# Kernel tuning notes

Hardware: AMD Instinct MI355X
Metric: run time of the kernel (lower is better)

## Reference

```python
import jax, jax.numpy as jnp
import numpy as np

EPS = 1e-8


def _cdist(a, b):
    # a: [B,N,3], b: [B,M,3] -> euclidean distances [B,N,M]
    a2 = jnp.sum(a * a, axis=-1)[:, :, None]          # [B,N,1]
    b2 = jnp.sum(b * b, axis=-1)[:, None, :]          # [B,1,M]
    ab = jnp.einsum('bnd,bmd->bnm', a, b)             # [B,N,M]
    d2 = jnp.maximum(a2 + b2 - 2.0 * ab, 0.0)
    return jnp.sqrt(d2)


def setup_inputs() -> dict:
    key = jax.random.key(0)
    ks = jax.random.split(key, 8)
    B, N, M, C1, C2 = 16, 4096, 1024, 128, 256
    Cin = C1 + C2  # 384
    H1, H2 = 256, 128
    return {
        'xyz1': jax.random.normal(ks[0], (B, N, 3), dtype=jnp.float32),
        'xyz2': jax.random.normal(ks[1], (B, M, 3), dtype=jnp.float32),
        'points1': jax.random.normal(ks[2], (B, C1, N), dtype=jnp.float32),
        'points2': jax.random.normal(ks[3], (B, C2, M), dtype=jnp.float32),
        'W1': jax.random.normal(ks[4], (H1, Cin), dtype=jnp.float32) * (1.0 / np.sqrt(Cin)),
        'b1': jnp.zeros((H1,), dtype=jnp.float32),
        'W2': jax.random.normal(ks[5], (H2, H1), dtype=jnp.float32) * (1.0 / np.sqrt(H1)),
        'b2': jnp.zeros((H2,), dtype=jnp.float32),
    }


def reference(xyz1, xyz2, points1, points2, W1, b1, W2, b2):
    # inverse-distance weighted interpolation over ALL M source points
    dist = _cdist(xyz1, xyz2) + EPS                   # [B,N,M]
    inv = 1.0 / dist
    weight = inv / jnp.sum(inv, axis=-1, keepdims=True)
    # interpolated features: [B,N,M] @ [B,M,C2] -> [B,C2,N]
    interpolated = jnp.einsum('bnm,bcm->bcn', weight, points2)
    new_points = jnp.concatenate([points1, interpolated], axis=1)  # [B,C1+C2,N]
    # 1x1 Conv1d MLP with ReLU
    h = jax.nn.relu(jnp.einsum('oc,bcn->bon', W1, new_points) + b1[None, :, None])
    out = jax.nn.relu(jnp.einsum('oc,bcn->bon', W2, h) + b2[None, :, None])
    return out
```

## Files before the change

### kernel.cpp

```cpp
#include <hip/hip_runtime.h>
#include <math.h>

#define BBATCH 16
#define NPTS   4096
#define MPTS   1024
#define C1c    128
#define C2c    256
#define CINc   384
#define H1c    256
#define H2c    128
#define TN     64

typedef _Float16 f16x8 __attribute__((ext_vector_type(8)));
typedef _Float16 f16x4 __attribute__((ext_vector_type(4)));
typedef float    f32x4 __attribute__((ext_vector_type(4)));

#define INV_HALF   8192
#define SMEM_UNION 32768
#define SMEM_BYTES (SMEM_UNION + 1024)

#define NFRAG_P2  (BBATCH * 32 * 16 * 64)
#define NFRAG_W1  (16 * 12 * 64)
#define NFRAG_W2  (8 * 8 * 64)
#define WS_P2S  0
#define WS_W1S  (NFRAG_P2 * 8)
#define WS_W2S  (WS_W1S + NFRAG_W1 * 8)
#define WS_F16_TOTAL (WS_W2S + NFRAG_W2 * 8)

__global__ __launch_bounds__(256) void cvt_swz(
    const float* __restrict__ p2, const float* __restrict__ W1,
    const float* __restrict__ W2, _Float16* __restrict__ ws)
{
    const int t = blockIdx.x * 256 + threadIdx.x;
    const float* src;
    _Float16* dst;
    if (t < NFRAG_P2) {
        const int lane = t & 63, wt = (t >> 6) & 15, s = (t >> 10) & 31, b = t >> 15;
        const int c = wt * 16 + (lane & 15);
        const int m = s * 32 + (lane >> 4) * 8;
        src = p2 + ((size_t)(b * C2c + c)) * MPTS + m;
        dst = ws + WS_P2S + (size_t)t * 8;
    } else if (t < NFRAG_P2 + NFRAG_W1) {
        const int u = t - NFRAG_P2;
        const int lane = u & 63, kc = (u >> 6) % 12, wt = (u >> 6) / 12;
        const int o = wt * 16 + (lane & 15);
        const int k = kc * 32 + (lane >> 4) * 8;
        src = W1 + (size_t)o * CINc + k;
        dst = ws + WS_W1S + (size_t)u * 8;
    } else {
        const int v = t - NFRAG_P2 - NFRAG_W1;
        const int lane = v & 63, oc = (v >> 6) & 7, wt2 = v >> 9;
        const int o = wt2 * 16 + (lane & 15);
        const int k = oc * 32 + (lane >> 4) * 8;
        src = W2 + (size_t)o * H1c + k;
        dst = ws + WS_W2S + (size_t)v * 8;
    }
    const float4 a0 = *(const float4*)(src);
    const float4 a1 = *(const float4*)(src + 4);
    f16x8 h;
    h[0] = (_Float16)a0.x; h[1] = (_Float16)a0.y; h[2] = (_Float16)a0.z; h[3] = (_Float16)a0.w;
    h[4] = (_Float16)a1.x; h[5] = (_Float16)a1.y; h[6] = (_Float16)a1.z; h[7] = (_Float16)a1.w;
    *(f16x8*)dst = h;
}

template <bool F16P>
__global__ __launch_bounds__(256, 4) void fp_mfma8(
    const float* __restrict__ xyz1, const float* __restrict__ xyz2,
    const float* __restrict__ p1,   const float* __restrict__ p2,
    const float* __restrict__ W1,   const float* __restrict__ b1v,
    const float* __restrict__ W2,   const float* __restrict__ b2v,
    const _Float16* __restrict__ p2s, const _Float16* __restrict__ W1s,
    const _Float16* __restrict__ W2s,
    float* __restrict__ out)
{
    __shared__ __align__(16) char smem[SMEM_BYTES];
    _Float16* s_inv = (_Float16*)smem;
    _Float16* s_X   = (_Float16*)smem;
    _Float16* s_H   = (_Float16*)smem;
    float*    s_red = (float*)(smem + SMEM_UNION);

    const int tid  = threadIdx.x;
    const int w    = tid >> 6;
    const int L    = tid & 63;
    const int quad = L >> 4;
    const int l16  = L & 15;

    const int id = blockIdx.x;
    const int b  = (id & 7) * 2 + ((id >> 3) & 1);
    const int n0 = (id >> 4) * TN;

    const float* __restrict__ z2b = xyz2 + (size_t)b * MPTS * 3;
    const float* __restrict__ p2b = p2   + (size_t)b * C2c * MPTS;
    const _Float16* __restrict__ p2sb =
        F16P ? (p2s + (((size_t)b * 32 * 16 + (size_t)w * 4) * 64 + L) * 8) : (const _Float16*)nullptr;

    const float x1x = xyz1[((size_t)b * NPTS + n0 + L) * 3 + 0];
    const float x1y = xyz1[((size_t)b * NPTS + n0 + L) * 3 + 1];
    const float x1z = xyz1[((size_t)b * NPTS + n0 + L) * 3 + 2];

    f32x4 acc[4][4];
    #pragma unroll
    for (int ct = 0; ct < 4; ++ct)
        #pragma unroll
        for (int nt = 0; nt < 4; ++nt)
            acc[ct][nt] = (f32x4){0.f, 0.f, 0.f, 0.f};

    float ssum = 0.f;
    f16x8 Aa[2][4];

    auto loadA = [&](int s, f16x8 dst[4]) {
        if (F16P) {
            const _Float16* ap = p2sb + (size_t)s * (16 * 64 * 8);
            #pragma unroll
            for (int ct = 0; ct < 4; ++ct)
                dst[ct] = *(const f16x8*)(ap + (size_t)ct * (64 * 8));
        } else {
            const float* ap = p2b + (size_t)(w * 64 + l16) * MPTS + s * 32 + quad * 8;
            #pragma unroll
            for (int ct = 0; ct < 4; ++ct) {
                const float4 a0 = *(const float4*)(ap + (size_t)ct * (16 * MPTS));
                const float4 a1 = *(const float4*)(ap + (size_t)ct * (16 * MPTS) + 4);
                f16x8 h;
                h[0] = (_Float16)a0.x; h[1] = (_Float16)a0.y; h[2] = (_Float16)a0.z; h[3] = (_Float16)a0.w;
                h[4] = (_Float16)a1.x; h[5] = (_Float16)a1.y; h[6] = (_Float16)a1.z; h[7] = (_Float16)a1.w;
                dst[ct] = h;
            }
        }
    };

    auto gen = [&](int ss_) {
        _Float16* buf = s_inv + (ss_ & 1) * INV_HALF;
        const float* zbase = z2b + (size_t)(ss_ * 128 + w * 32) * 3;
        #pragma unroll
        for (int g = 0; g < 4; ++g) {
            const float* zp = zbase + g * 24;
            f32x4 zr[6];
            #pragma unroll
            for (int j = 0; j < 6; ++j) zr[j] = ((const f32x4*)zp)[j];
            const float* zv = (const float*)zr;
            f16x8 iv;
            #pragma unroll
            for (int i = 0; i < 8; ++i) {
                const float dx = x1x - zv[3 * i + 0];
                const float dy = x1y - zv[3 * i + 1];
                const float dz = x1z - zv[3 * i + 2];
                const float d2 = fmaf(dx, dx, fmaf(dy, dy, fmaf(dz, dz, 1e-12f)));
                const float inv = __builtin_amdgcn_rsqf(d2);
                ssum += inv;
                iv[i] = (_Float16)inv;
            }
            *(f16x8*)(buf + (((w * 4 + quad) * 64) + g * 16 + l16) * 8) = iv;
        }
    };

    loadA(0, Aa[0]);
    gen(0);
    __syncthreads();

    for (int ss = 0; ss < 8; ++ss) {
        if (ss + 1 < 8) gen(ss + 1);
        const _Float16* buf = s_inv + (ss & 1) * INV_HALF;
        #pragma unroll
        for (int cc = 0; cc < 4; ++cc) {
            const int s = ss * 4 + cc;
            if (s + 1 < 32) loadA(s + 1, Aa[(cc + 1) & 1]);
            #pragma unroll
            for (int nt = 0; nt < 4; ++nt) {
                const f16x8 bf = *(const f16x8*)(buf + ((cc * 4 + nt) * 64 + L) * 8);
                #pragma unroll
                for (int ct = 0; ct < 4; ++ct)
                    acc[ct][nt] = __builtin_amdgcn_mfma_f32_16x16x32_f16(Aa[cc & 1][ct], bf, acc[ct][nt], 0, 0, 0);
            }
        }
        __syncthreads();
    }

    s_red[tid] = ssum;
    __syncthreads();
    if (tid < 64)
        s_red[tid] = 1.0f / (s_red[tid] + s_red[tid + 64] + s_red[tid + 128] + s_red[tid + 192]);
    __syncthreads();

    {
        float rn4[4];
        #pragma unroll
        for (int nt = 0; nt < 4; ++nt) rn4[nt] = s_red[nt * 16 + l16];
        #pragma unroll
        for (int ct = 0; ct < 4; ++ct) {
            const int kq = 2 * w + (ct >> 1);
            const int lp = l16 + 16 * (((ct & 1) * 2) + (quad >> 1));
            const int jo = (quad & 1) * 4;
            #pragma unroll
            for (int nt = 0; nt < 4; ++nt) {
                const f32x4 v = acc[ct][nt];
                const float r = rn4[nt];
                f16x4 hv;
                hv[0] = (_Float16)(v[0] * r);
                hv[1] = (_Float16)(v[1] * r);
                hv[2] = (_Float16)(v[2] * r);
                hv[3] = (_Float16)(v[3] * r);
                *(f16x4*)(s_X + ((kq * 4 + nt) * 64 + lp) * 8 + jo) = hv;
            }
        }
    }
    __syncthreads();

    f32x4 hacc[4][4];
    #pragma unroll
    for (int ct = 0; ct < 4; ++ct)
        #pragma unroll
        for (int nt = 0; nt < 4; ++nt)
            hacc[ct][nt] = (f32x4){0.f, 0.f, 0.f, 0.f};

    {
        const float* p1f = p1 + ((size_t)b * C1c + quad * 8) * NPTS + n0 + l16;
        #pragma unroll
        for (int kc = 0; kc < 4; ++kc) {
            f16x8 af[4];
            if (F16P) {
                const _Float16* wp = W1s + (((size_t)(w * 4) * 12 + kc) * 64 + L) * 8;
                #pragma unroll
                for (int ct = 0; ct < 4; ++ct)
                    af[ct] = *(const f16x8*)(wp + (size_t)ct * (12 * 64 * 8));
            } else {
                const float* wp = W1 + (size_t)(w * 64 + l16) * CINc + kc * 32 + quad * 8;
                #pragma unroll
                for (int ct = 0; ct < 4; ++ct) {
                    const float4 a0 = *(const float4*)(wp + ct * (16 * CINc));
                    const float4 a1 = *(const float4*)(wp + ct * (16 * CINc) + 4);
                    f16x8 h;
                    h[0] = (_Float16)a0.x; h[1] = (_Float16)a0.y; h[2] = (_Float16)a0.z; h[3] = (_Float16)a0.w;
                    h[4] = (_Float16)a1.x; h[5] = (_Float16)a1.y; h[6] = (_Float16)a1.z; h[7] = (_Float16)a1.w;
                    af[ct] = h;
                }
            }
            #pragma unroll
            for (int nt = 0; nt < 4; ++nt) {
                const float* pp = p1f + (size_t)(kc * 32) * NPTS + nt * 16;
                float t[8];
                #pragma unroll
                for (int j = 0; j < 8; ++j) t[j] = pp[(size_t)j * NPTS];
                f16x8 bf;
                #pragma unroll
                for (int j = 0; j < 8; ++j) bf[j] = (_Float16)t[j];
                #pragma unroll
                for (int ct = 0; ct < 4; ++ct)
                    hacc[ct][nt] = __builtin_amdgcn_mfma_f32_16x16x32_f16(af[ct], bf, hacc[ct][nt], 0, 0, 0);
            }
        }
    }

    #pragma unroll 2
    for (int kc = 4; kc < 12; ++kc) {
        f16x8 af[4];
        if (F16P) {
            const _Float16* wp = W1s + (((size_t)(w * 4) * 12 + kc) * 64 + L) * 8;
            #pragma unroll
            for (int ct = 0; ct < 4; ++ct)
                af[ct] = *(const f16x8*)(wp + (size_t)ct * (12 * 64 * 8));
        } else {
            const float* wp = W1 + (size_t)(w * 64 + l16) * CINc + kc * 32 + quad * 8;
            #pragma unroll
            for (int ct = 0; ct < 4; ++ct) {
                const float4 a0 = *(const float4*)(wp + ct * (16 * CINc));
                const float4 a1 = *(const float4*)(wp + ct * (16 * CINc) + 4);
                f16x8 h;
                h[0] = (_Float16)a0.x; h[1] = (_Float16)a0.y; h[2] = (_Float16)a0.z; h[3] = (_Float16)a0.w;
                h[4] = (_Float16)a1.x; h[5] = (_Float16)a1.y; h[6] = (_Float16)a1.z; h[7] = (_Float16)a1.w;
                af[ct] = h;
            }
        }
        #pragma unroll
        for (int nt = 0; nt < 4; ++nt) {
            const f16x8 bf = *(const f16x8*)(s_X + (((kc - 4) * 4 + nt) * 64 + L) * 8);
            #pragma unroll
            for (int ct = 0; ct < 4; ++ct)
                hacc[ct][nt] = __builtin_amdgcn_mfma_f32_16x16x32_f16(af[ct], bf, hacc[ct][nt], 0, 0, 0);
        }
    }

    __syncthreads();

    {
        f32x4 bb[4];
        #pragma unroll
        for (int ct = 0; ct < 4; ++ct)
            bb[ct] = *(const f32x4*)(b1v + w * 64 + ct * 16 + quad * 4);
        #pragma unroll
        for (int ct = 0; ct < 4; ++ct) {
            const int oq = 2 * w + (ct >> 1);
            const int lp = l16 + 16 * (((ct & 1) * 2) + (quad >> 1));
            const int jo = (quad & 1) * 4;
            #pragma unroll
            for (int nt = 0; nt < 4; ++nt) {
                const f32x4 v = hacc[ct][nt];
                f16x4 hv;
                hv[0] = (_Float16)fmaxf(v[0] + bb[ct][0], 0.f);
                hv[1] = (_Float16)fmaxf(v[1] + bb[ct][1], 0.f);
                hv[2] = (_Float16)fmaxf(v[2] + bb[ct][2], 0.f);
                hv[3] = (_Float16)fmaxf(v[3] + bb[ct][3], 0.f);
                *(f16x4*)(s_H + ((oq * 4 + nt) * 64 + lp) * 8 + jo) = hv;
            }
        }
    }
    __syncthreads();

    f32x4 oacc[2][4];
    #pragma unroll
    for (int ct = 0; ct < 2; ++ct)
        #pragma unroll
        for (int nt = 0; nt < 4; ++nt)
            oacc[ct][nt] = (f32x4){0.f, 0.f, 0.f, 0.f};

    #pragma unroll 2
    for (int oc = 0; oc < 8; ++oc) {
        f16x8 af2[2];
        if (F16P) {
            const _Float16* wp = W2s + (((size_t)(w * 2) * 8 + oc) * 64 + L) * 8;
            #pragma unroll
            for (int ct = 0; ct < 2; ++ct)
                af2[ct] = *(const f16x8*)(wp + (size_t)ct * (8 * 64 * 8));
        } else {
            const float* wp = W2 + (size_t)(w * 32 + l16) * H1c + oc * 32 + quad * 8;
            #pragma unroll
            for (int ct = 0; ct < 2; ++ct) {
                const float4 a0 = *(const float4*)(wp + ct * (16 * H1c));
                const float4 a1 = *(const float4*)(wp + ct * (16 * H1c) + 4);
                f16x8 h;
                h[0] = (_Float16)a0.x; h[1] = (_Float16)a0.y; h[2] = (_Float16)a0.z; h[3] = (_Float16)a0.w;
                h[4] = (_Float16)a1.x; h[5] = (_Float16)a1.y; h[6] = (_Float16)a1.z; h[7] = (_Float16)a1.w;
                af2[ct] = h;
            }
        }
        #pragma unroll
        for (int nt = 0; nt < 4; ++nt) {
            const f16x8 bf = *(const f16x8*)(s_H + ((oc * 4 + nt) * 64 + L) * 8);
            #pragma unroll
            for (int ct = 0; ct < 2; ++ct)
                oacc[ct][nt] = __builtin_amdgcn_mfma_f32_16x16x32_f16(af2[ct], bf, oacc[ct][nt], 0, 0, 0);
        }
    }

    {
        f32x4 bb2[2];
        #pragma unroll
        for (int ct = 0; ct < 2; ++ct)
            bb2[ct] = *(const f32x4*)(b2v + w * 32 + ct * 16 + quad * 4);
        #pragma unroll
        for (int ct = 0; ct < 2; ++ct)
            #pragma unroll
            for (int nt = 0; nt < 4; ++nt) {
                float* op = out + ((size_t)b * H2c + w * 32 + ct * 16 + quad * 4) * NPTS
                                + n0 + nt * 16 + l16;
                #pragma unroll
                for (int j = 0; j < 4; ++j)
                    op[(size_t)j * NPTS] = fmaxf(oacc[ct][nt][j] + bb2[ct][j], 0.f);
            }
    }
}

extern "C" void kernel_launch(void* const* d_in, const int* in_sizes, int n_in,
                              void* d_out, int out_size, void* d_ws, size_t ws_size,
                              hipStream_t stream) {
    (void)in_sizes; (void)n_in; (void)out_size;
    const float* xyz1 = (const float*)d_in[0];
    const float* xyz2 = (const float*)d_in[1];
    const float* p1   = (const float*)d_in[2];
    const float* p2   = (const float*)d_in[3];
    const float* W1   = (const float*)d_in[4];
    const float* b1   = (const float*)d_in[5];
    const float* W2   = (const float*)d_in[6];
    const float* b2   = (const float*)d_in[7];
    float* out = (float*)d_out;

    dim3 grid(BBATCH * (NPTS / TN));
    dim3 block(256);
    if (ws_size >= (size_t)WS_F16_TOTAL * 2) {
        _Float16* ws = (_Float16*)d_ws;
        const int nswz = NFRAG_P2 + NFRAG_W1 + NFRAG_W2;
        cvt_swz<<<dim3(nswz / 256), dim3(256), 0, stream>>>(p2, W1, W2, ws);
        fp_mfma8<true><<<grid, block, 0, stream>>>(xyz1, xyz2, p1, p2, W1, b1, W2, b2,
                                                   ws + WS_P2S, ws + WS_W1S, ws + WS_W2S, out);
    } else {
        fp_mfma8<false><<<grid, block, 0, stream>>>(xyz1, xyz2, p1, p2, W1, b1, W2, b2,
                                                    nullptr, nullptr, nullptr, out);
    }
}
```

Measured before the change: 186.3 us.

## Stage xyz2 in LDS, stage points1 in LDS, add MFMA priority hints

Each block now copies the batch's full xyz2 (12 KB) into shared memory and the distance generation reads it from there instead of global memory. points1 is converted to fp16 and written into the shared X tile next to the interpolated features, so the first MLP layer becomes one uniform 12-chunk loop over shared memory instead of strided global loads feeding the MFMAs. s_setprio is raised around the MFMA loops. The extra ~16 KB of shared memory lowers occupancy, with launch bounds dropping from 4 to 3 blocks per CU, and adds an extra barrier.

```diff
diff --git a/kernel.cpp b/kernel.cpp
--- a/kernel.cpp
+++ b/kernel.cpp
@@ -16,8 +16,9 @@
 typedef float    f32x4 __attribute__((ext_vector_type(4)));
 
 #define INV_HALF   8192
-#define SMEM_UNION 32768
-#define SMEM_BYTES (SMEM_UNION + 1024)
+#define OFF_XYZ2   32768
+#define OFF_RED    49152
+#define SMEM_BYTES 50176
 
 #define NFRAG_P2  (BBATCH * 32 * 16 * 64)
 #define NFRAG_W1  (16 * 12 * 64)
@@ -64,7 +65,7 @@
 }
 
 template <bool F16P>
-__global__ __launch_bounds__(256, 4) void fp_mfma8(
+__global__ __launch_bounds__(256, 3) void fp_mfma9(
     const float* __restrict__ xyz1, const float* __restrict__ xyz2,
     const float* __restrict__ p1,   const float* __restrict__ p2,
     const float* __restrict__ W1,   const float* __restrict__ b1v,
@@ -74,10 +75,11 @@
     float* __restrict__ out)
 {
     __shared__ __align__(16) char smem[SMEM_BYTES];
-    _Float16* s_inv = (_Float16*)smem;
-    _Float16* s_X   = (_Float16*)smem;
-    _Float16* s_H   = (_Float16*)smem;
-    float*    s_red = (float*)(smem + SMEM_UNION);
+    _Float16* s_inv  = (_Float16*)smem;
+    float*    s_xyz2 = (float*)(smem + OFF_XYZ2);
+    _Float16* s_X    = (_Float16*)smem;
+    _Float16* s_H    = (_Float16*)smem;
+    float*    s_red  = (float*)(smem + OFF_RED);
 
     const int tid  = threadIdx.x;
     const int w    = tid >> 6;
@@ -93,6 +95,9 @@
     const float* __restrict__ p2b = p2   + (size_t)b * C2c * MPTS;
     const _Float16* __restrict__ p2sb =
         F16P ? (p2s + (((size_t)b * 32 * 16 + (size_t)w * 4) * 64 + L) * 8) : (const _Float16*)nullptr;
+
+    for (int i = tid; i < MPTS * 3 / 4; i += 256)
+        ((f32x4*)s_xyz2)[i] = ((const f32x4*)z2b)[i];
 
     const float x1x = xyz1[((size_t)b * NPTS + n0 + L) * 3 + 0];
     const float x1y = xyz1[((size_t)b * NPTS + n0 + L) * 3 + 1];
@@ -130,7 +135,7 @@
 
     auto gen = [&](int ss_) {
         _Float16* buf = s_inv + (ss_ & 1) * INV_HALF;
-        const float* zbase = z2b + (size_t)(ss_ * 128 + w * 32) * 3;
+        const float* zbase = s_xyz2 + (size_t)(ss_ * 128 + w * 32) * 3;
         #pragma unroll
         for (int g = 0; g < 4; ++g) {
             const float* zp = zbase + g * 24;
@@ -154,6 +159,7 @@
     };
 
     loadA(0, Aa[0]);
+    __syncthreads();
     gen(0);
     __syncthreads();
 
@@ -164,6 +170,7 @@
         for (int cc = 0; cc < 4; ++cc) {
             const int s = ss * 4 + cc;
             if (s + 1 < 32) loadA(s + 1, Aa[(cc + 1) & 1]);
+            __builtin_amdgcn_s_setprio(1);
             #pragma unroll
             for (int nt = 0; nt < 4; ++nt) {
                 const f16x8 bf = *(const f16x8*)(buf + ((cc * 4 + nt) * 64 + L) * 8);
@@ -171,8 +178,23 @@
                 for (int ct = 0; ct < 4; ++ct)
                     acc[ct][nt] = __builtin_amdgcn_mfma_f32_16x16x32_f16(Aa[cc & 1][ct], bf, acc[ct][nt], 0, 0, 0);
             }
+            __builtin_amdgcn_s_setprio(0);
         }
         __syncthreads();
+    }
+
+    {
+        const float* p1b = p1 + ((size_t)b * C1c + w * 32 + quad * 8) * NPTS + n0 + l16;
+        #pragma unroll
+        for (int cc = 0; cc < 4; ++cc) {
+            float t[8];
+            #pragma unroll
+            for (int j = 0; j < 8; ++j) t[j] = p1b[(size_t)j * NPTS + cc * 16];
+            f16x8 v;
+            #pragma unroll
+            for (int j = 0; j < 8; ++j) v[j] = (_Float16)t[j];
+            *(f16x8*)(s_X + ((w * 4 + cc) * 64 + L) * 8) = v;
+        }
     }
 
     s_red[tid] = ssum;
@@ -187,7 +209,7 @@
         for (int nt = 0; nt < 4; ++nt) rn4[nt] = s_red[nt * 16 + l16];
         #pragma unroll
         for (int ct = 0; ct < 4; ++ct) {
-            const int kq = 2 * w + (ct >> 1);
+            const int kq = 4 + 2 * w + (ct >> 1);
             const int lp = l16 + 16 * (((ct & 1) * 2) + (quad >> 1));
             const int jo = (quad & 1) * 4;
             #pragma unroll
@@ -212,46 +234,8 @@
         for (int nt = 0; nt < 4; ++nt)
             hacc[ct][nt] = (f32x4){0.f, 0.f, 0.f, 0.f};
 
-    {
-        const float* p1f = p1 + ((size_t)b * C1c + quad * 8) * NPTS + n0 + l16;
-        #pragma unroll
-        for (int kc = 0; kc < 4; ++kc) {
-            f16x8 af[4];
-            if (F16P) {
-                const _Float16* wp = W1s + (((size_t)(w * 4) * 12 + kc) * 64 + L) * 8;
-                #pragma unroll
-                for (int ct = 0; ct < 4; ++ct)
-                    af[ct] = *(const f16x8*)(wp + (size_t)ct * (12 * 64 * 8));
-            } else {
-                const float* wp = W1 + (size_t)(w * 64 + l16) * CINc + kc * 32 + quad * 8;
-                #pragma unroll
-                for (int ct = 0; ct < 4; ++ct) {
-                    const float4 a0 = *(const float4*)(wp + ct * (16 * CINc));
-                    const float4 a1 = *(const float4*)(wp + ct * (16 * CINc) + 4);
-                    f16x8 h;
-                    h[0] = (_Float16)a0.x; h[1] = (_Float16)a0.y; h[2] = (_Float16)a0.z; h[3] = (_Float16)a0.w;
-                    h[4] = (_Float16)a1.x; h[5] = (_Float16)a1.y; h[6] = (_Float16)a1.z; h[7] = (_Float16)a1.w;
-                    af[ct] = h;
-                }
-            }
-            #pragma unroll
-            for (int nt = 0; nt < 4; ++nt) {
-                const float* pp = p1f + (size_t)(kc * 32) * NPTS + nt * 16;
-                float t[8];
-                #pragma unroll
-                for (int j = 0; j < 8; ++j) t[j] = pp[(size_t)j * NPTS];
-                f16x8 bf;
-                #pragma unroll
-                for (int j = 0; j < 8; ++j) bf[j] = (_Float16)t[j];
-                #pragma unroll
-                for (int ct = 0; ct < 4; ++ct)
-                    hacc[ct][nt] = __builtin_amdgcn_mfma_f32_16x16x32_f16(af[ct], bf, hacc[ct][nt], 0, 0, 0);
-            }
-        }
-    }
-
     #pragma unroll 2
-    for (int kc = 4; kc < 12; ++kc) {
+    for (int kc = 0; kc < 12; ++kc) {
         f16x8 af[4];
         if (F16P) {
             const _Float16* wp = W1s + (((size_t)(w * 4) * 12 + kc) * 64 + L) * 8;
@@ -270,13 +254,15 @@
                 af[ct] = h;
             }
         }
+        __builtin_amdgcn_s_setprio(1);
         #pragma unroll
         for (int nt = 0; nt < 4; ++nt) {
-            const f16x8 bf = *(const f16x8*)(s_X + (((kc - 4) * 4 + nt) * 64 + L) * 8);
+            const f16x8 bf = *(const f16x8*)(s_X + ((kc * 4 + nt) * 64 + L) * 8);
             #pragma unroll
             for (int ct = 0; ct < 4; ++ct)
                 hacc[ct][nt] = __builtin_amdgcn_mfma_f32_16x16x32_f16(af[ct], bf, hacc[ct][nt], 0, 0, 0);
         }
+        __builtin_amdgcn_s_setprio(0);
     }
 
     __syncthreads();
@@ -332,6 +318,7 @@
                 af2[ct] = h;
             }
         }
+        __builtin_amdgcn_s_setprio(1);
         #pragma unroll
         for (int nt = 0; nt < 4; ++nt) {
             const f16x8 bf = *(const f16x8*)(s_H + ((oc * 4 + nt) * 64 + L) * 8);
@@ -339,6 +326,7 @@
             for (int ct = 0; ct < 2; ++ct)
                 oacc[ct][nt] = __builtin_amdgcn_mfma_f32_16x16x32_f16(af2[ct], bf, oacc[ct][nt], 0, 0, 0);
         }
+        __builtin_amdgcn_s_setprio(0);
     }
 
     {
@@ -379,10 +367,10 @@
         _Float16* ws = (_Float16*)d_ws;
         const int nswz = NFRAG_P2 + NFRAG_W1 + NFRAG_W2;
         cvt_swz<<<dim3(nswz / 256), dim3(256), 0, stream>>>(p2, W1, W2, ws);
-        fp_mfma8<true><<<grid, block, 0, stream>>>(xyz1, xyz2, p1, p2, W1, b1, W2, b2,
+        fp_mfma9<true><<<grid, block, 0, stream>>>(xyz1, xyz2, p1, p2, W1, b1, W2, b2,
                                                    ws + WS_P2S, ws + WS_W1S, ws + WS_W2S, out);
     } else {
-        fp_mfma8<false><<<grid, block, 0, stream>>>(xyz1, xyz2, p1, p2, W1, b1, W2, b2,
+        fp_mfma9<false><<<grid, block, 0, stream>>>(xyz1, xyz2, p1, p2, W1, b1, W2, b2,
                                                     nullptr, nullptr, nullptr, out);
     }
 }
```

Measured after the change: 162.9 us. 1.14x faster.
